# Kernel tuning notes

Hardware: AMD Instinct MI355X
Metric: run time of the kernel (lower is better)

Reference implementation:

```python
import jax, jax.numpy as jnp
import numpy as np
from jax import lax

V, H, B, S, T = 32000, 512, 32, 256, 16  # vocab, hidden, batch, src_len, keyword_len


def setup_inputs() -> dict:
    key = jax.random.key(0)
    ks = jax.random.split(key, 26)
    sc = 0.02
    def P(k, *shape):
        return jax.random.normal(k, shape, jnp.float32) * sc
    return {
        "theme": jax.random.randint(ks[0], (1, B), 0, V),
        "keyword": jax.random.randint(ks[1], (T, B), 0, V),
        "src": jax.random.randint(ks[2], (S, B), 0, V),
        "theme_tab": P(ks[3], V, H),
        "keyword_tab": P(ks[4], V, H),
        "src_tab": P(ks[5], V, H),
        # GRU params (PyTorch layout: W_ih/W_hh are (3H, H) stacked r,z,n)
        "Wih_f": P(ks[6], 3 * H, H), "Whh_f": P(ks[7], 3 * H, H),
        "bih_f": P(ks[8], 3 * H), "bhh_f": P(ks[9], 3 * H),
        "Wih_b": P(ks[10], 3 * H, H), "Whh_b": P(ks[11], 3 * H, H),
        "bih_b": P(ks[12], 3 * H), "bhh_b": P(ks[13], 3 * H),
        # Linear layers (PyTorch layout: W is (out, in))
        "Ww": P(ks[14], H, 2 * H), "bw": P(ks[15], H),      # enc_w_weight
        "Wt": P(ks[16], H, H), "bt": P(ks[17], H),          # enc_theme_weight
        "Wk": P(ks[18], H, H), "bk": P(ks[19], H),          # enc_keyword_weight
        "wv": P(ks[20], H), "bv": P(ks[21]),                # enc_weight (H -> 1)
        "Wo": P(ks[22], H, 3 * H), "bo": P(ks[23], H),      # enc_output_out
        "Who": P(ks[24], H, 2 * H),                         # enc_hidden_out (no bias)
    }


def _gru_dir(x, Wih, Whh, bih, bhh, reverse):
    # x: (S, B, H). Returns (outputs (S,B,H), final hidden (B,H)).
    h = Whh.shape[1]
    gx = jnp.einsum('sbh,gh->sbg', x, Wih) + bih  # precompute input gates for all steps
    if reverse:
        gx = gx[::-1]
    h0 = jnp.zeros((x.shape[1], h), x.dtype)

    def step(hprev, g):
        gh = hprev @ Whh.T + bhh
        xr, xz, xn = jnp.split(g, 3, axis=-1)
        hr, hz, hn = jnp.split(gh, 3, axis=-1)
        r = jax.nn.sigmoid(xr + hr)
        z = jax.nn.sigmoid(xz + hz)
        n = jnp.tanh(xn + r * hn)
        hnew = (1.0 - z) * n + z * hprev
        return hnew, hnew

    hT, ys = lax.scan(step, h0, gx)
    if reverse:
        ys = ys[::-1]
    return ys, hT


def _forward(theme, keyword, src,
             theme_tab, keyword_tab, src_tab,
             Wih_f, Whh_f, bih_f, bhh_f,
             Wih_b, Whh_b, bih_b, bhh_b,
             Ww, bw, Wt, bt, Wk, bk, wv, bv, Wo, bo, Who):
    hdim = Whh_f.shape[1]
    src_emb = src_tab[src]          # (S, B, H)
    theme_emb = theme_tab[theme]    # (1, B, H)
    keyword_emb = keyword_tab[keyword]  # (T, B, H)

    ys_f, hT_f = _gru_dir(src_emb, Wih_f, Whh_f, bih_f, bhh_f, reverse=False)
    ys_b, hT_b = _gru_dir(src_emb, Wih_b, Whh_b, bih_b, bhh_b, reverse=True)
    enc_output = jnp.concatenate([ys_f, ys_b], axis=-1)   # (S, B, 2H); == enc_w_1 (the split/cat is identity)
    enc_hidden = jnp.concatenate([hT_f, hT_b], axis=-1)[None]  # (1, B, 2H)

    enc_w_1 = enc_output.transpose(1, 0, 2)     # (B, S, 2H)
    enc_theme = theme_emb.transpose(1, 0, 2)    # (B, 1, H)
    enc_keyword = keyword_emb.transpose(1, 0, 2)  # (B, T, H)

    # point(): additive-attention broadcast scoring
    b1 = enc_w_1 @ Ww.T + bw                    # (B, S, H)
    theme_proj = enc_theme[:, 0, :] @ Wt.T + bt  # (B, H)  == b22
    b3 = enc_keyword @ Wk.T + bk                # (B, T, H)
    b4 = jnp.tanh(b1[:, :, None, :] + theme_proj[:, None, None, :] + b3[:, None, :, :])  # (B,S,T,H)
    scores = b4 @ wv + bv                        # (B, S, T)
    enc_w_2 = jnp.einsum('bst,bh->bsh', scores, theme_proj)  # bmm(scores, b22 broadcast over T)

    concat_enc_w = jnp.concatenate([enc_w_2, enc_w_1], axis=-1)  # (B, S, 3H)
    enc_out = (concat_enc_w @ Wo.T + bo).transpose(1, 0, 2)      # (S, B, H)
    enc_hidden_out = enc_hidden @ Who.T                          # (1, B, H)
    return enc_out, enc_hidden_out


def reference(theme, keyword, src,
              theme_tab, keyword_tab, src_tab,
              Wih_f, Whh_f, bih_f, bhh_f,
              Wih_b, Whh_b, bih_b, bhh_b,
              Ww, bw, Wt, bt, Wk, bk, wv, bv, Wo, bo, Who):
    return _forward(theme, keyword, src,
                    theme_tab, keyword_tab, src_tab,
                    Wih_f, Whh_f, bih_f, bhh_f,
                    Wih_b, Whh_b, bih_b, bhh_b,
                    Ww, bw, Wt, bt, Wk, bk, wv, bv, Wo, bo, Who)
```

## Files before the change

kernel.cpp:

```cpp
#include <hip/hip_runtime.h>

typedef unsigned short u16;
typedef unsigned long long u64;
typedef __attribute__((ext_vector_type(8))) short bf16x8;
typedef __attribute__((ext_vector_type(4))) float f32x4;

__device__ __forceinline__ float bf2f(u16 u) {
  union { unsigned int i; float f; } v; v.i = ((unsigned int)u) << 16; return v.f;
}
__device__ __forceinline__ u16 f2bf(float f) {
  union { float f; unsigned int i; } v; v.f = f;
  unsigned int r = (v.i + 0x7FFFu + ((v.i >> 16) & 1u)) >> 16;
  return (u16)r;
}
__device__ __forceinline__ float sigmoidf_(float x) { return 1.f / (1.f + __expf(-x)); }
__device__ __forceinline__ float tanhf_(float x) {
  x = fminf(fmaxf(x, -10.f), 10.f);
  float e2 = __expf(2.f * x);
  return (e2 - 1.f) / (e2 + 1.f);
}

static const size_t OFF_GX    = 0;
static const size_t OFF_HBUF  = 50331648;
static const size_t OFF_ASRC  = 67174400;
static const size_t OFF_EW1   = 75563008;
static const size_t OFF_B1    = 92340224;
static const size_t OFF_WIHC  = 109117440;
static const size_t OFF_WWB   = 112263168;
static const size_t OFF_WO2B  = 113311744;
static const size_t OFF_WKB   = 114360320;
static const size_t OFF_KWE   = 114884608;
static const size_t OFF_B3    = 115408896;
static const size_t OFF_TP    = 116457472;
static const size_t OFF_TPO   = 116523008;
static const size_t OFF_SSUM  = 116588544;
static const size_t OFF_BIASC = 116621312;
static const size_t OFF_FLG   = 116633600;
static const size_t OFF_CLM   = 116666496;

__global__ __launch_bounds__(256) void cvtk(const float* __restrict__ s,
                                            u16* __restrict__ d, int n) {
  int i = (blockIdx.x * 256 + threadIdx.x) * 4;
  if (i < n) {
    float4 v = *(const float4*)(s + i);
    ushort4 o; o.x = f2bf(v.x); o.y = f2bf(v.y); o.z = f2bf(v.z); o.w = f2bf(v.w);
    *(ushort4*)(d + i) = o;
  }
}

__global__ __launch_bounds__(256) void cvt_wo2(const float* __restrict__ Wo,
                                               u16* __restrict__ d) {
  int i = (blockIdx.x * 256 + threadIdx.x) * 4;
  int nrow = i >> 10, c = i & 1023;
  float4 v = *(const float4*)(Wo + (size_t)nrow * 1536 + 512 + c);
  ushort4 o; o.x = f2bf(v.x); o.y = f2bf(v.y); o.z = f2bf(v.z); o.w = f2bf(v.w);
  *(ushort4*)(d + i) = o;
}

__global__ __launch_bounds__(256) void gather_rows(const int* __restrict__ ids,
                                                   const float* __restrict__ tab,
                                                   u16* __restrict__ dst, int mode) {
  int i = (blockIdx.x * 256 + threadIdx.x) * 8;
  int r = i >> 9, c = i & 511;
  int id = (mode == 0) ? ids[r] : ids[((r & 15) << 5) + (r >> 4)];
  const float* s = tab + (size_t)id * 512 + c;
  alignas(16) u16 o[8];
#pragma unroll
  for (int j = 0; j < 8; ++j) o[j] = f2bf(s[j]);
  *(uint4*)(dst + i) = *(const uint4*)o;
}

__global__ __launch_bounds__(256) void proj_tp(const int* __restrict__ theme,
                                               const float* __restrict__ tab,
                                               const float* __restrict__ W,
                                               const float* __restrict__ bias,
                                               float* __restrict__ outp) {
  int o = blockIdx.x * 256 + threadIdx.x;
  int b = o >> 9, n = o & 511;
  const float* emb = tab + (size_t)theme[b] * 512;
  const float* wr = W + (size_t)n * 512;
  float acc = 0.f;
  for (int h = 0; h < 512; h += 4) {
    float4 e = *(const float4*)(emb + h);
    float4 w = *(const float4*)(wr + h);
    acc += e.x * w.x + e.y * w.y + e.z * w.z + e.w * w.w;
  }
  outp[o] = acc + bias[n];
}

__global__ __launch_bounds__(256) void proj_tpo(const float* __restrict__ tp,
                                                const float* __restrict__ Wo,
                                                float* __restrict__ outp) {
  int o = blockIdx.x * 256 + threadIdx.x;
  int b = o >> 9, n = o & 511;
  const float* emb = tp + (size_t)b * 512;
  const float* wr = Wo + (size_t)n * 1536;
  float acc = 0.f;
  for (int h = 0; h < 512; h += 4) {
    float4 e = *(const float4*)(emb + h);
    float4 w = *(const float4*)(wr + h);
    acc += e.x * w.x + e.y * w.y + e.z * w.z + e.w * w.w;
  }
  outp[o] = acc;
}

template <int EPI>
__global__ __launch_bounds__(256) void gemm_bt(const u16* __restrict__ A,
                                               const u16* __restrict__ B,
                                               const float* __restrict__ bias,
                                               float* __restrict__ Cf,
                                               u16* __restrict__ Cb, int M, int N,
                                               int K, const float* __restrict__ ssum,
                                               const float* __restrict__ tpo) {
  __shared__ u16 As[128][72];
  __shared__ u16 Bs[128][72];
  const int tid = threadIdx.x;
  const int mtiles = M >> 7;
  const int mt = blockIdx.x % mtiles, nt = blockIdx.x / mtiles;
  const int wave = tid >> 6, lane = tid & 63;
  const int wr = wave >> 1, wc = wave & 1;
  const int l16 = lane & 15, l4 = lane >> 4;
  f32x4 acc[4][4] = {};
  const int nkt = K >> 6;
  for (int kt = 0; kt < nkt; ++kt) {
    __syncthreads();
#pragma unroll
    for (int i = 0; i < 4; ++i) {
      int c = i * 256 + tid;
      int row = c >> 3, c8 = c & 7;
      uint4 va = *(const uint4*)(A + (size_t)(mt * 128 + row) * K + kt * 64 + c8 * 8);
      *(uint4*)&As[row][c8 * 8] = va;
      uint4 vb = *(const uint4*)(B + (size_t)(nt * 128 + row) * K + kt * 64 + c8 * 8);
      *(uint4*)&Bs[row][c8 * 8] = vb;
    }
    __syncthreads();
#pragma unroll
    for (int kk = 0; kk < 2; ++kk) {
      bf16x8 af[4], bfr[4];
#pragma unroll
      for (int m = 0; m < 4; ++m)
        af[m] = *(const bf16x8*)&As[wr * 64 + m * 16 + l16][kk * 32 + l4 * 8];
#pragma unroll
      for (int n = 0; n < 4; ++n)
        bfr[n] = *(const bf16x8*)&Bs[wc * 64 + n * 16 + l16][kk * 32 + l4 * 8];
#pragma unroll
      for (int m = 0; m < 4; ++m)
#pragma unroll
        for (int n = 0; n < 4; ++n)
          acc[m][n] = __builtin_amdgcn_mfma_f32_16x16x32_bf16(af[m], bfr[n],
                                                              acc[m][n], 0, 0, 0);
    }
  }
#pragma unroll
  for (int m = 0; m < 4; ++m) {
    int rg = mt * 128 + wr * 64 + m * 16 + l4 * 4;
#pragma unroll
    for (int n = 0; n < 4; ++n) {
      int cg = nt * 128 + wc * 64 + n * 16 + l16;
      float bb = bias[cg];
#pragma unroll
      for (int i = 0; i < 4; ++i) {
        int r = rg + i;
        float v = acc[m][n][i] + bb;
        if (EPI == 2) v += ssum[r] * tpo[(r & 31) * 512 + cg];
        if (EPI == 0) Cb[(size_t)r * N + cg] = f2bf(v);
        else Cf[(size_t)r * N + cg] = v;
      }
    }
  }
}

__global__ __launch_bounds__(512, 1) void gru_scan(
    const u16* __restrict__ gx,
    const float* __restrict__ Whh_f, const float* __restrict__ Whh_b,
    const float* __restrict__ bhh_f, const float* __restrict__ bhh_b,
    u16* __restrict__ hbuf,
    int* __restrict__ flg,
    int* __restrict__ clm)
{
  __shared__ float pbuf[4][3][4][64];
  __shared__ int sInfo[2];
  const int tid = threadIdx.x;

  int xcc;
  asm volatile("s_getreg_b32 %0, hwreg(HW_REG_XCC_ID)" : "=s"(xcc));
  xcc &= 7;
  if (tid == 0) {
    int r = __hip_atomic_fetch_add(&clm[xcc], 1, __ATOMIC_RELAXED,
                                   __HIP_MEMORY_SCOPE_AGENT);
    sInfo[0] = r;
    if (r == 31) {
      int exp = 0;
      __hip_atomic_compare_exchange_strong(&clm[8], &exp, xcc + 1,
                                           __ATOMIC_RELAXED, __ATOMIC_RELAXED,
                                           __HIP_MEMORY_SCOPE_AGENT);
    }
    int c;
    do {
      c = __hip_atomic_load(&clm[8], __ATOMIC_RELAXED, __HIP_MEMORY_SCOPE_AGENT);
      if (c == 0) __builtin_amdgcn_s_sleep(8);
    } while (c == 0);
    sInfo[1] = c - 1;
  }
  __syncthreads();
  const int rank = sInfo[0];
  if (sInfo[1] != xcc || rank >= 32) return;

  const int d = rank & 1;
  const int slice = rank >> 1;
  const float* Whh = d ? Whh_b : Whh_f;
  const float* bhh = d ? bhh_b : bhh_f;

  const int wave = tid >> 6, lane = tid & 63;
  const int kh = wave >> 2, m = (wave >> 1) & 1, a = wave & 1;
  const int p = m * 2 + a;
  const int l16 = lane & 15, l4 = lane >> 4;
  const int j = a * 16 + l16;

  bf16x8 wfrag[3][8];
#pragma unroll
  for (int g = 0; g < 3; ++g) {
    const float* wrow = Whh + (size_t)(g * 512 + slice * 32 + j) * 512;
#pragma unroll
    for (int kk = 0; kk < 8; ++kk) {
      const float* wp = wrow + (kh * 8 + kk) * 32 + l4 * 8;
      float4 v0 = *(const float4*)wp;
      float4 v1 = *(const float4*)(wp + 4);
      alignas(16) u16 tmp[8];
      tmp[0] = f2bf(v0.x); tmp[1] = f2bf(v0.y); tmp[2] = f2bf(v0.z); tmp[3] = f2bf(v0.w);
      tmp[4] = f2bf(v1.x); tmp[5] = f2bf(v1.y); tmp[6] = f2bf(v1.z); tmp[7] = f2bf(v1.w);
      wfrag[g][kk] = *(const bf16x8*)tmp;
    }
  }
  float bR = 0.f, bZ = 0.f, bN = 0.f;
  if (kh == 0) {
    bR = bhh[slice * 32 + j];
    bZ = bhh[512 + slice * 32 + j];
    bN = bhh[1024 + slice * 32 + j];
  }
  float hreg[4] = {0.f, 0.f, 0.f, 0.f};

  const size_t dbase = (size_t)d * 257 * 32 * 512;
  int* const flgd = flg + (size_t)d * 257 * 16;

  for (int t = 0; t < 256; ++t) {
    float xg[3][4];
    if (kh == 0) {
      int trow = d ? (255 - t) : t;
      const u16* gb = gx + (size_t)(trow * 32 + m * 16 + l4 * 4) * 3072 +
                      d * 1536 + slice * 32 + j;
#pragma unroll
      for (int i = 0; i < 4; ++i)
#pragma unroll
        for (int g = 0; g < 3; ++g)
          xg[g][i] = bf2f(gb[(size_t)i * 3072 + g * 512]);
      __builtin_amdgcn_sched_barrier(0);
    }

    if (t > 0) {
      if (wave == 0) {
        const int* fp = flgd + (size_t)t * 16 + l16;
        while (true) {
          int v = __hip_atomic_load(fp, __ATOMIC_RELAXED, __HIP_MEMORY_SCOPE_AGENT);
          if (__all(v != 0)) break;
        }
      }
      __builtin_amdgcn_fence(__ATOMIC_ACQUIRE, "workgroup");
      __syncthreads();
    }

    const u16* hsrc = hbuf + dbase + (size_t)t * 32 * 512 +
                      (size_t)(m * 16 + l16) * 512 + kh * 256 + l4 * 8;
    uint4 areg[8];
#pragma unroll
    for (int kk = 0; kk < 8; ++kk)
      areg[kk] = *(const uint4*)(hsrc + kk * 32);

    f32x4 acc[3] = {};
#pragma unroll
    for (int kk = 0; kk < 8; ++kk) {
      union { uint4 u; bf16x8 v; } cv;
      cv.u = areg[kk];
#pragma unroll
      for (int g = 0; g < 3; ++g)
        acc[g] = __builtin_amdgcn_mfma_f32_16x16x32_bf16(cv.v, wfrag[g][kk],
                                                         acc[g], 0, 0, 0);
    }

    if (kh == 1) {
#pragma unroll
      for (int g = 0; g < 3; ++g)
#pragma unroll
        for (int i = 0; i < 4; ++i) pbuf[p][g][i][lane] = acc[g][i];
    }
    __syncthreads();

    if (kh == 0) {
      u16* hrow = hbuf + dbase + (size_t)(t + 1) * 32 * 512 + slice * 32;
#pragma unroll
      for (int i = 0; i < 4; ++i) {
        float hr = acc[0][i] + pbuf[p][0][i][lane] + bR;
        float hz = acc[1][i] + pbuf[p][1][i][lane] + bZ;
        float hn = acc[2][i] + pbuf[p][2][i][lane] + bN;
        float rr = sigmoidf_(xg[0][i] + hr);
        float zz = sigmoidf_(xg[1][i] + hz);
        float nn = tanhf_(xg[2][i] + rr * hn);
        hreg[i] = (1.f - zz) * nn + zz * hreg[i];
      }
#pragma unroll
      for (int i = 0; i < 4; ++i) {
        unsigned int myb = f2bf(hreg[i]);
        unsigned int ob = (unsigned int)__shfl_xor((int)myb, 1);
        if ((l16 & 1) == 0) {
          unsigned int w = (myb & 0xffffu) | (ob << 16);
          unsigned int* dst = (unsigned int*)(hrow +
                              (size_t)(m * 16 + l4 * 4 + i) * 512 + j);
          __hip_atomic_store(dst, w, __ATOMIC_RELAXED, __HIP_MEMORY_SCOPE_AGENT);
        }
      }
    }
    asm volatile("s_waitcnt vmcnt(0)" ::: "memory");
    __syncthreads();
    if (tid == 0)
      __hip_atomic_store(flgd + (size_t)(t + 1) * 16 + slice, 1,
                         __ATOMIC_RELAXED, __HIP_MEMORY_SCOPE_AGENT);
  }
}

__global__ __launch_bounds__(256) void build_encw1(const u16* __restrict__ hbuf,
                                                   u16* __restrict__ ew) {
  int idx = (blockIdx.x * 256 + threadIdx.x) * 8;
  int r = idx >> 10, c = idx & 1023;
  int s = r >> 5, b = r & 31;
  size_t src;
  if (c < 512) src = ((size_t)(s + 1) * 32 + b) * 512 + c;
  else src = ((size_t)(257 + 256 - s) * 32 + b) * 512 + (c - 512);
  *(uint4*)(ew + idx) = *(const uint4*)(hbuf + src);
}

__global__ __launch_bounds__(256) void scores_k(const float* __restrict__ b1,
                                                const float* __restrict__ tp,
                                                const float* __restrict__ b3,
                                                const float* __restrict__ wv,
                                                const float* __restrict__ bv,
                                                float* __restrict__ ssum) {
  __shared__ float pre[512];
  __shared__ float wvs[512];
  __shared__ float red[4];
  int r = blockIdx.x;
  int tid = threadIdx.x;
  int b = r & 31;
  for (int h = tid; h < 512; h += 256) {
    pre[h] = b1[(size_t)r * 512 + h] + tp[b * 512 + h];
    wvs[h] = wv[h];
  }
  __syncthreads();
  float acc = 0.f;
  for (int t = 0; t < 16; ++t) {
    const float* b3r = b3 + ((size_t)b * 16 + t) * 512;
    for (int h = tid; h < 512; h += 256) acc += wvs[h] * tanhf_(pre[h] + b3r[h]);
  }
  for (int o = 32; o > 0; o >>= 1) acc += __shfl_down(acc, o);
  if ((tid & 63) == 0) red[tid >> 6] = acc;
  __syncthreads();
  if (tid == 0) ssum[r] = red[0] + red[1] + red[2] + red[3] + 16.f * bv[0];
}

__global__ __launch_bounds__(256) void hidden_k(const u16* __restrict__ hbuf,
                                                const float* __restrict__ Who,
                                                float* __restrict__ outp) {
  int o = blockIdx.x * 256 + threadIdx.x;
  int b = o >> 9, n = o & 511;
  const u16* hf = hbuf + ((size_t)256 * 32 + b) * 512;
  const u16* hb = hbuf + ((size_t)(257 + 256) * 32 + b) * 512;
  const float* w = Who + (size_t)n * 1024;
  float acc = 0.f;
  for (int k = 0; k < 512; ++k) acc += bf2f(hf[k]) * w[k];
  for (int k = 0; k < 512; ++k) acc += bf2f(hb[k]) * w[512 + k];
  outp[o] = acc;
}

extern "C" void kernel_launch(void* const* d_in, const int* in_sizes, int n_in,
                              void* d_out, int out_size, void* d_ws, size_t ws_size,
                              hipStream_t stream) {
  (void)in_sizes; (void)n_in; (void)out_size; (void)ws_size;
  const int* theme = (const int*)d_in[0];
  const int* keyword = (const int*)d_in[1];
  const int* src = (const int*)d_in[2];
  const float* theme_tab = (const float*)d_in[3];
  const float* keyword_tab = (const float*)d_in[4];
  const float* src_tab = (const float*)d_in[5];
  const float* Wih_f = (const float*)d_in[6];
  const float* Whh_f = (const float*)d_in[7];
  const float* bih_f = (const float*)d_in[8];
  const float* bhh_f = (const float*)d_in[9];
  const float* Wih_b = (const float*)d_in[10];
  const float* Whh_b = (const float*)d_in[11];
  const float* bih_b = (const float*)d_in[12];
  const float* bhh_b = (const float*)d_in[13];
  const float* Ww = (const float*)d_in[14];
  const float* bw = (const float*)d_in[15];
  const float* Wt = (const float*)d_in[16];
  const float* bt = (const float*)d_in[17];
  const float* Wk = (const float*)d_in[18];
  const float* bk = (const float*)d_in[19];
  const float* wv = (const float*)d_in[20];
  const float* bv = (const float*)d_in[21];
  const float* Wo = (const float*)d_in[22];
  const float* bo = (const float*)d_in[23];
  const float* Who = (const float*)d_in[24];
  float* out = (float*)d_out;
  char* ws = (char*)d_ws;

  u16* gx_cat = (u16*)(ws + OFF_GX);
  u16* hbuf = (u16*)(ws + OFF_HBUF);
  u16* asrc = (u16*)(ws + OFF_ASRC);
  u16* ew1 = (u16*)(ws + OFF_EW1);
  float* b1buf = (float*)(ws + OFF_B1);
  u16* wihc = (u16*)(ws + OFF_WIHC);
  u16* wwb = (u16*)(ws + OFF_WWB);
  u16* wo2b = (u16*)(ws + OFF_WO2B);
  u16* wkb = (u16*)(ws + OFF_WKB);
  u16* kwe = (u16*)(ws + OFF_KWE);
  float* b3buf = (float*)(ws + OFF_B3);
  float* tp = (float*)(ws + OFF_TP);
  float* tpo = (float*)(ws + OFF_TPO);
  float* ssum = (float*)(ws + OFF_SSUM);
  float* biasc = (float*)(ws + OFF_BIASC);
  int* flg = (int*)(ws + OFF_FLG);
  int* clm = (int*)(ws + OFF_CLM);

  hipMemsetAsync(flg, 0, 2 * 257 * 16 * 4 + 64, stream);
  hipMemsetAsync(hbuf, 0, 32 * 512 * 2, stream);
  hipMemsetAsync(hbuf + (size_t)257 * 32 * 512, 0, 32 * 512 * 2, stream);
  hipMemcpyAsync(biasc, bih_f, 1536 * 4, hipMemcpyDeviceToDevice, stream);
  hipMemcpyAsync(biasc + 1536, bih_b, 1536 * 4, hipMemcpyDeviceToDevice, stream);

  cvtk<<<768, 256, 0, stream>>>(Wih_f, wihc, 1536 * 512);
  cvtk<<<768, 256, 0, stream>>>(Wih_b, wihc + 1536 * 512, 1536 * 512);
  cvtk<<<512, 256, 0, stream>>>(Ww, wwb, 512 * 1024);
  cvtk<<<256, 256, 0, stream>>>(Wk, wkb, 512 * 512);
  cvt_wo2<<<512, 256, 0, stream>>>(Wo, wo2b);
  gather_rows<<<2048, 256, 0, stream>>>(src, src_tab, asrc, 0);
  gather_rows<<<128, 256, 0, stream>>>(keyword, keyword_tab, kwe, 1);
  proj_tp<<<64, 256, 0, stream>>>(theme, theme_tab, Wt, bt, tp);
  proj_tpo<<<64, 256, 0, stream>>>(tp, Wo, tpo);
  gemm_bt<1><<<16, 256, 0, stream>>>(kwe, wkb, bk, b3buf, nullptr, 512, 512, 512,
                                     nullptr, nullptr);
  gemm_bt<0><<<1536, 256, 0, stream>>>(asrc, wihc, biasc, nullptr, gx_cat, 8192,
                                       3072, 512, nullptr, nullptr);
  gru_scan<<<256, 512, 0, stream>>>(gx_cat, Whh_f, Whh_b, bhh_f, bhh_b, hbuf, flg,
                                    clm);
  build_encw1<<<4096, 256, 0, stream>>>(hbuf, ew1);
  gemm_bt<1><<<256, 256, 0, stream>>>(ew1, wwb, bw, b1buf, nullptr, 8192, 512, 1024,
                                      nullptr, nullptr);
  scores_k<<<8192, 256, 0, stream>>>(b1buf, tp, b3buf, wv, bv, ssum);
  gemm_bt<2><<<256, 256, 0, stream>>>(ew1, wo2b, bo, out, nullptr, 8192, 512, 1024,
                                      ssum, tpo);
  hidden_k<<<64, 256, 0, stream>>>(hbuf, Who, out + 4194304);
}
```

Baseline: 1.304 ms.

## Use per-wave flags and double-buffered LDS to cut barriers in GRU scan

The GRU scan now signals step completion with one flag per producing wave (64 flags per step) instead of one per block. Every wave polls the flags itself, so the block-wide barrier after the poll and the end-of-step barrier are removed. The partial-sum LDS buffer is double-buffered by step parity so that only the single mid-step barrier is needed. The next step's input-gate loads are prefetched right after the flag store, and a large dummy LDS allocation forces one block per CU. The flag area is moved into the b1 buffer region. The risks are more polling traffic on the flags and reliance on the reuse of the b1 region being safe at that point in the pipeline.

```diff
diff --git a/kernel.cpp b/kernel.cpp
--- a/kernel.cpp
+++ b/kernel.cpp
@@ -35,8 +35,8 @@
 static const size_t OFF_TPO   = 116523008;
 static const size_t OFF_SSUM  = 116588544;
 static const size_t OFF_BIASC = 116621312;
-static const size_t OFF_FLG   = 116633600;
-static const size_t OFF_CLM   = 116666496;
+static const size_t OFF_FLG   = OFF_B1;
+static const size_t OFF_CLM   = OFF_B1 + 131584;
 
 __global__ __launch_bounds__(256) void cvtk(const float* __restrict__ s,
                                             u16* __restrict__ d, int n) {
@@ -178,8 +178,9 @@
     int* __restrict__ flg,
     int* __restrict__ clm)
 {
-  __shared__ float pbuf[4][3][4][64];
+  __shared__ float pbuf[2][4][3][4][64];
   __shared__ int sInfo[2];
+  __shared__ char ldspad[65536];
   const int tid = threadIdx.x;
 
   int xcc;
@@ -204,6 +205,10 @@
   }
   __syncthreads();
   const int rank = sInfo[0];
+  if (rank > 1000000) {
+    ldspad[tid] = (char)rank;
+    clm[24] = ldspad[(tid * 7) & 65535];
+  }
   if (sInfo[1] != xcc || rank >= 32) return;
 
   const int d = rank & 1;
@@ -241,32 +246,27 @@
   float hreg[4] = {0.f, 0.f, 0.f, 0.f};
 
   const size_t dbase = (size_t)d * 257 * 32 * 512;
-  int* const flgd = flg + (size_t)d * 257 * 16;
+  int* const flgd = flg + (size_t)d * 257 * 64;
+
+  float xg[3][4];
+  if (kh == 0) {
+    const u16* gb = gx + (size_t)((d ? 255 : 0) * 32 + m * 16 + l4 * 4) * 3072 +
+                    d * 1536 + slice * 32 + j;
+#pragma unroll
+    for (int i = 0; i < 4; ++i)
+#pragma unroll
+      for (int g = 0; g < 3; ++g)
+        xg[g][i] = bf2f(gb[(size_t)i * 3072 + g * 512]);
+  }
 
   for (int t = 0; t < 256; ++t) {
-    float xg[3][4];
-    if (kh == 0) {
-      int trow = d ? (255 - t) : t;
-      const u16* gb = gx + (size_t)(trow * 32 + m * 16 + l4 * 4) * 3072 +
-                      d * 1536 + slice * 32 + j;
-#pragma unroll
-      for (int i = 0; i < 4; ++i)
-#pragma unroll
-        for (int g = 0; g < 3; ++g)
-          xg[g][i] = bf2f(gb[(size_t)i * 3072 + g * 512]);
-      __builtin_amdgcn_sched_barrier(0);
-    }
-
     if (t > 0) {
-      if (wave == 0) {
-        const int* fp = flgd + (size_t)t * 16 + l16;
-        while (true) {
-          int v = __hip_atomic_load(fp, __ATOMIC_RELAXED, __HIP_MEMORY_SCOPE_AGENT);
-          if (__all(v != 0)) break;
-        }
+      const int* fp = flgd + (size_t)t * 64 + lane;
+      while (true) {
+        int v = __hip_atomic_load(fp, __ATOMIC_RELAXED, __HIP_MEMORY_SCOPE_AGENT);
+        if (__all(v != 0)) break;
       }
       __builtin_amdgcn_fence(__ATOMIC_ACQUIRE, "workgroup");
-      __syncthreads();
     }
 
     const u16* hsrc = hbuf + dbase + (size_t)t * 32 * 512 +
@@ -291,7 +291,7 @@
 #pragma unroll
       for (int g = 0; g < 3; ++g)
 #pragma unroll
-        for (int i = 0; i < 4; ++i) pbuf[p][g][i][lane] = acc[g][i];
+        for (int i = 0; i < 4; ++i) pbuf[t & 1][p][g][i][lane] = acc[g][i];
     }
     __syncthreads();
 
@@ -299,9 +299,9 @@
       u16* hrow = hbuf + dbase + (size_t)(t + 1) * 32 * 512 + slice * 32;
 #pragma unroll
       for (int i = 0; i < 4; ++i) {
-        float hr = acc[0][i] + pbuf[p][0][i][lane] + bR;
-        float hz = acc[1][i] + pbuf[p][1][i][lane] + bZ;
-        float hn = acc[2][i] + pbuf[p][2][i][lane] + bN;
+        float hr = acc[0][i] + pbuf[t & 1][p][0][i][lane] + bR;
+        float hz = acc[1][i] + pbuf[t & 1][p][1][i][lane] + bZ;
+        float hn = acc[2][i] + pbuf[t & 1][p][2][i][lane] + bN;
         float rr = sigmoidf_(xg[0][i] + hr);
         float zz = sigmoidf_(xg[1][i] + hz);
         float nn = tanhf_(xg[2][i] + rr * hn);
@@ -318,12 +318,21 @@
           __hip_atomic_store(dst, w, __ATOMIC_RELAXED, __HIP_MEMORY_SCOPE_AGENT);
         }
       }
-    }
-    asm volatile("s_waitcnt vmcnt(0)" ::: "memory");
-    __syncthreads();
-    if (tid == 0)
-      __hip_atomic_store(flgd + (size_t)(t + 1) * 16 + slice, 1,
-                         __ATOMIC_RELAXED, __HIP_MEMORY_SCOPE_AGENT);
+      asm volatile("s_waitcnt vmcnt(0)" ::: "memory");
+      if (lane == 0)
+        __hip_atomic_store(flgd + (size_t)(t + 1) * 64 + slice * 4 + p, 1,
+                           __ATOMIC_RELAXED, __HIP_MEMORY_SCOPE_AGENT);
+      if (t + 1 < 256) {
+        int trow = d ? (255 - (t + 1)) : (t + 1);
+        const u16* gb = gx + (size_t)(trow * 32 + m * 16 + l4 * 4) * 3072 +
+                        d * 1536 + slice * 32 + j;
+#pragma unroll
+        for (int i = 0; i < 4; ++i)
+#pragma unroll
+          for (int g = 0; g < 3; ++g)
+            xg[g][i] = bf2f(gb[(size_t)i * 3072 + g * 512]);
+      }
+    }
   }
 }
 
@@ -430,7 +439,7 @@
   int* flg = (int*)(ws + OFF_FLG);
   int* clm = (int*)(ws + OFF_CLM);
 
-  hipMemsetAsync(flg, 0, 2 * 257 * 16 * 4 + 64, stream);
+  hipMemsetAsync(flg, 0, 131584 + 128, stream);
   hipMemsetAsync(hbuf, 0, 32 * 512 * 2, stream);
   hipMemsetAsync(hbuf + (size_t)257 * 32 * 512, 0, 32 * 512 * 2, stream);
   hipMemcpyAsync(biasc, bih_f, 1536 * 4, hipMemcpyDeviceToDevice, stream);
```

New measurement: 2.501 ms. 91.7% more time.
